# Performance work log

Measured on AMD Instinct MI355X. Metric: run time of the kernel, lower is better.

Reference implementation:

```python
import jax, jax.numpy as jnp
import numpy as np

TIME_STEPS = 49      # time_steps init arg
NUM_STEPS = 5000     # (time_steps+1)/dt = max_solve_steps
DT = 0.01            # dt0 in diffeqsolve
B = 8192             # batch of independent simulations


def setup_inputs() -> dict:
    key = jax.random.key(0)
    k1, k2, k3 = jax.random.split(key, 3)
    # positive, well-conditioned rates in [0.05, 0.5)
    condition = 0.05 + 0.45 * jax.random.uniform(k1, (B, 4), dtype=jnp.float32)
    # standard normals; scaled by sqrt(dt) inside reference -> Brownian increments
    dW = jax.random.normal(k2, (NUM_STEPS, B), dtype=jnp.float32)
    # uniform jitter used in summarize()'s max_at
    u = jax.random.uniform(k3, (B,), dtype=jnp.float32)
    return {"condition": condition, "dW": dW, "u": u}


def _simulate(condition, dW):
    # condition columns: infection_rate, recovery_rate, r0_mean_reversion, r0_volatility
    inf_rate = condition[:, 0]
    rec = condition[:, 1]
    mr = condition[:, 2]
    vol = condition[:, 3]
    r0_init = inf_rate / rec
    b = condition.shape[0]
    y0 = jnp.stack([
        jnp.full((b,), 0.99, condition.dtype),  # S
        jnp.full((b,), 0.01, condition.dtype),  # I
        jnp.zeros((b,), condition.dtype),       # R
        r0_init,                                # R0
    ], axis=-1)  # [B,4]
    sqrt_dt = jnp.sqrt(jnp.asarray(DT, condition.dtype))

    def step(y, dw):
        s, i, r, r0 = y[:, 0], y[:, 1], y[:, 2], y[:, 3]
        newly_infected = r0 * rec * s
        newly_recovered = rec * i
        # Euler-Maruyama: drift * dt + diffusion * dW, diffusion only on R0,
        # scaled by sqrt(|R0|) as in sde()
        y_new = jnp.stack([
            s - DT * newly_infected,
            i + DT * (newly_infected - newly_recovered),
            r + DT * newly_recovered,
            r0 + DT * mr * (r0_init - r0) + jnp.sqrt(jnp.abs(r0)) * vol * (dw * sqrt_dt),
        ], axis=-1)
        return y_new, y_new[:, 1]  # carry full state, emit infected fraction

    _, infected = jax.lax.scan(step, y0, dW)  # infected: [NUM_STEPS, B]
    # SaveAt ts = 1..TIME_STEPS: step k ends at t=(k+1)*DT, so t=m is index 100*m-1
    x = infected[99:100 * TIME_STEPS:100]  # [TIME_STEPS, B]
    return jnp.nan_to_num(x, nan=0.0, posinf=0.0, neginf=0.0)


def reference(condition, dW, u):
    x = _simulate(condition, dW)          # [T, B] infected trajectories
    x = jnp.clip(x, 1e-5)
    max_ = x.max(axis=0)
    max_at = (jnp.argmax(x, axis=0).astype(x.dtype) + u) / TIME_STEPS
    vol = jnp.std(jnp.diff(jnp.log(x), axis=0), axis=0)
    return jnp.stack([max_, max_at, vol], axis=-1)  # [B, 3]
```

## Files before the change

kernel.cpp:

```cpp
#include <hip/hip_runtime.h>
#include <math.h>

#define BATCH 8192
#define TPB   32
#define SEGN  25

#define REP25(M) M(0) M(1) M(2) M(3) M(4) M(5) M(6) M(7) M(8) M(9) \
  M(10) M(11) M(12) M(13) M(14) M(15) M(16) M(17) M(18) M(19) \
  M(20) M(21) M(22) M(23) M(24)

#define DECL_A(k) float a##k;
#define DECL_B(k) float b##k;
#define LD_A(k)   a##k = pA[(size_t)(k) * BATCH];
#define LD_B(k)   b##k = pB[(size_t)(k) * BATCH];

#define STEP_BODY(dwv) { \
    float dw  = (dwv); \
    float pr  = dtrec * r0; \
    float ps  = pr * s; \
    float r0a = r0 * c1 + c2; \
    float sq  = sqrtf(fabsf(r0)); \
    float g   = dw * volc; \
    s  = s - ps; \
    i_ = i_ * ci + ps; \
    r0 = r0a + sq * g; }

#define STEP_A(k) STEP_BODY(a##k)
#define STEP_B(k) STEP_BODY(b##k)

__global__ __launch_bounds__(TPB, 1)
void sir_sde_kernel(const float* __restrict__ cond,
                    const float* __restrict__ dW,
                    const float* __restrict__ uu,
                    float* __restrict__ out)
{
    const int b = blockIdx.x * TPB + threadIdx.x;

    const float inf_rate = cond[b * 4 + 0];
    const float rec      = cond[b * 4 + 1];
    const float mr       = cond[b * 4 + 2];
    const float vol      = cond[b * 4 + 3];

    const float dt    = 0.01f;
    const float r0i   = inf_rate / rec;
    const float dtrec = dt * rec;
    const float ci    = 1.0f - dtrec;
    const float c1    = 1.0f - dt * mr;
    const float c2    = (dt * mr) * r0i;
    const float volc  = vol * sqrtf(dt);

    float s  = 0.99f;
    float i_ = 0.01f;
    float r0 = r0i;

    float maxv = -1.0f, maxat = 0.0f;
    float prevlx = 0.0f, sum = 0.0f, sumsq = 0.0f;
    int   reccount = 0;

    REP25(DECL_A)
    REP25(DECL_B)

    const float* dWb = dW + b;
    const float* pA  = dWb;
    const float* pB;

    REP25(LD_A)

    for (int sg = 0; sg < 196; sg += 2) {
        pB = dWb + (size_t)(sg + 1) * SEGN * BATCH;
        __builtin_amdgcn_sched_barrier(0);
        REP25(LD_B)
        __builtin_amdgcn_sched_barrier(0);

        REP25(STEP_A)

        pA = dWb + (size_t)((sg + 2 < 196) ? sg + 2 : 0) * SEGN * BATCH;
        __builtin_amdgcn_sched_barrier(0);
        REP25(LD_A)
        __builtin_amdgcn_sched_barrier(0);

        REP25(STEP_B)

        if ((sg & 3) == 2) {
            float x = __builtin_isfinite(i_) ? i_ : 0.0f;
            x = fmaxf(x, 1e-5f);
            float lx = logf(x);
            if (reccount > 0) {
                float d = lx - prevlx;
                sum   += d;
                sumsq += d * d;
            }
            prevlx = lx;
            if (x > maxv) { maxv = x; maxat = (float)reccount; }
            ++reccount;
        }
    }

    float mean = sum / 48.0f;
    float var  = sumsq / 48.0f - mean * mean;
    var = fmaxf(var, 0.0f);
    float volout    = sqrtf(var);
    float maxat_out = (maxat + uu[b]) / 49.0f;

    out[b * 3 + 0] = maxv;
    out[b * 3 + 1] = maxat_out;
    out[b * 3 + 2] = volout;
}

extern "C" void kernel_launch(void* const* d_in, const int* in_sizes, int n_in,
                              void* d_out, int out_size, void* d_ws, size_t ws_size,
                              hipStream_t stream)
{
    (void)in_sizes; (void)n_in; (void)out_size; (void)d_ws; (void)ws_size;
    const float* cond = (const float*)d_in[0];
    const float* dW   = (const float*)d_in[1];
    const float* uu   = (const float*)d_in[2];
    float* out = (float*)d_out;

    dim3 grid(BATCH / TPB), block(TPB);
    hipLaunchKernelGGL(sir_sde_kernel, grid, block, 0, stream, cond, dW, uu, out);
}
```

Before: 625.6 us.

## Double segment size and hand-issue dW prefetch loads with explicit vmcnt waits

Each prefetch segment grows from 25 to 50 time steps. The dW loads are now issued through inline-asm global_load_dword with a scalar base and an incrementing vector offset, and explicit s_waitcnt vmcnt(50) makes the kernel wait only for the older batch while the newer 50 loads stay in flight. The record and stat update now runs once per 100-step iteration instead of behind a modulo test, and the u load is hoisted to kernel start. The aim is to hide global-memory latency better and avoid compiler-inserted conservative waits in a latency-bound serial recurrence. The cost is more VGPR pressure and fragile hand-managed waitcnt semantics.

```diff
diff --git a/kernel.cpp b/kernel.cpp
--- a/kernel.cpp
+++ b/kernel.cpp
@@ -3,16 +3,58 @@
 
 #define BATCH 8192
 #define TPB   32
-#define SEGN  25
+#define SEG   50
 
-#define REP25(M) M(0) M(1) M(2) M(3) M(4) M(5) M(6) M(7) M(8) M(9) \
+
+#define REP50(M) M(0) M(1) M(2) M(3) M(4) M(5) M(6) M(7) M(8) M(9) \
   M(10) M(11) M(12) M(13) M(14) M(15) M(16) M(17) M(18) M(19) \
-  M(20) M(21) M(22) M(23) M(24)
+  M(20) M(21) M(22) M(23) M(24) M(25) M(26) M(27) M(28) M(29) \
+  M(30) M(31) M(32) M(33) M(34) M(35) M(36) M(37) M(38) M(39) \
+  M(40) M(41) M(42) M(43) M(44) M(45) M(46) M(47) M(48) M(49)
 
-#define DECL_A(k) float a##k;
-#define DECL_B(k) float b##k;
-#define LD_A(k)   a##k = pA[(size_t)(k) * BATCH];
-#define LD_B(k)   b##k = pB[(size_t)(k) * BATCH];
+#define DECL_A(k) float A##k = 0.0f;
+#define DECL_B(k) float B##k = 0.0f;
+
+#define LDL(k) "global_load_dword %[d" #k "], %[ob], %[sb]\n\t" \
+               "v_add_u32 %[ob], 0x8000, %[ob]\n\t"
+
+#define LD25 LDL(0) LDL(1) LDL(2) LDL(3) LDL(4) LDL(5) LDL(6) LDL(7) \
+  LDL(8) LDL(9) LDL(10) LDL(11) LDL(12) LDL(13) LDL(14) LDL(15) LDL(16) \
+  LDL(17) LDL(18) LDL(19) LDL(20) LDL(21) LDL(22) LDL(23) LDL(24)
+
+#define LOAD_LO(P) asm volatile(LD25 \
+  : [d0]"=v"(P##0),[d1]"=v"(P##1),[d2]"=v"(P##2),[d3]"=v"(P##3), \
+    [d4]"=v"(P##4),[d5]"=v"(P##5),[d6]"=v"(P##6),[d7]"=v"(P##7), \
+    [d8]"=v"(P##8),[d9]"=v"(P##9),[d10]"=v"(P##10),[d11]"=v"(P##11), \
+    [d12]"=v"(P##12),[d13]"=v"(P##13),[d14]"=v"(P##14),[d15]"=v"(P##15), \
+    [d16]"=v"(P##16),[d17]"=v"(P##17),[d18]"=v"(P##18),[d19]"=v"(P##19), \
+    [d20]"=v"(P##20),[d21]"=v"(P##21),[d22]"=v"(P##22),[d23]"=v"(P##23), \
+    [d24]"=v"(P##24),[ob]"+v"(ob) \
+  : [sb]"s"(dWp))
+
+#define LOAD_HI(P) asm volatile(LD25 \
+  : [d0]"=v"(P##25),[d1]"=v"(P##26),[d2]"=v"(P##27),[d3]"=v"(P##28), \
+    [d4]"=v"(P##29),[d5]"=v"(P##30),[d6]"=v"(P##31),[d7]"=v"(P##32), \
+    [d8]"=v"(P##33),[d9]"=v"(P##34),[d10]"=v"(P##35),[d11]"=v"(P##36), \
+    [d12]"=v"(P##37),[d13]"=v"(P##38),[d14]"=v"(P##39),[d15]"=v"(P##40), \
+    [d16]"=v"(P##41),[d17]"=v"(P##42),[d18]"=v"(P##43),[d19]"=v"(P##44), \
+    [d20]"=v"(P##45),[d21]"=v"(P##46),[d22]"=v"(P##47),[d23]"=v"(P##48), \
+    [d24]"=v"(P##49),[ob]"+v"(ob) \
+  : [sb]"s"(dWp))
+
+#define WAIT_LO(P) asm volatile("s_waitcnt vmcnt(50)" \
+  : "+v"(P##0),"+v"(P##1),"+v"(P##2),"+v"(P##3),"+v"(P##4), \
+    "+v"(P##5),"+v"(P##6),"+v"(P##7),"+v"(P##8),"+v"(P##9), \
+    "+v"(P##10),"+v"(P##11),"+v"(P##12),"+v"(P##13),"+v"(P##14), \
+    "+v"(P##15),"+v"(P##16),"+v"(P##17),"+v"(P##18),"+v"(P##19), \
+    "+v"(P##20),"+v"(P##21),"+v"(P##22),"+v"(P##23),"+v"(P##24))
+
+#define WAIT_HI(P) asm volatile("s_waitcnt vmcnt(50)" \
+  : "+v"(P##25),"+v"(P##26),"+v"(P##27),"+v"(P##28),"+v"(P##29), \
+    "+v"(P##30),"+v"(P##31),"+v"(P##32),"+v"(P##33),"+v"(P##34), \
+    "+v"(P##35),"+v"(P##36),"+v"(P##37),"+v"(P##38),"+v"(P##39), \
+    "+v"(P##40),"+v"(P##41),"+v"(P##42),"+v"(P##43),"+v"(P##44), \
+    "+v"(P##45),"+v"(P##46),"+v"(P##47),"+v"(P##48),"+v"(P##49))
 
 #define STEP_BODY(dwv) { \
     float dw  = (dwv); \
@@ -25,10 +67,11 @@
     i_ = i_ * ci + ps; \
     r0 = r0a + sq * g; }
 
-#define STEP_A(k) STEP_BODY(a##k)
-#define STEP_B(k) STEP_BODY(b##k)
+#define STEP_A(k) STEP_BODY(A##k)
+#define STEP_B(k) STEP_BODY(B##k)
 
-__global__ __launch_bounds__(TPB, 1)
+__global__ __attribute__((amdgpu_flat_work_group_size(TPB, TPB),
+                          amdgpu_waves_per_eu(1, 1)))
 void sir_sde_kernel(const float* __restrict__ cond,
                     const float* __restrict__ dW,
                     const float* __restrict__ uu,
@@ -36,6 +79,7 @@
 {
     const int b = blockIdx.x * TPB + threadIdx.x;
 
+    const float u_in     = uu[b];
     const float inf_rate = cond[b * 4 + 0];
     const float rec      = cond[b * 4 + 1];
     const float mr       = cond[b * 4 + 2];
@@ -57,31 +101,27 @@
     float prevlx = 0.0f, sum = 0.0f, sumsq = 0.0f;
     int   reccount = 0;
 
-    REP25(DECL_A)
-    REP25(DECL_B)
+    REP50(DECL_A)
+    REP50(DECL_B)
 
-    const float* dWb = dW + b;
-    const float* pA  = dWb;
-    const float* pB;
+    const float* dWp = dW;
+    unsigned ob = (unsigned)b * 4u;
 
-    REP25(LD_A)
+    LOAD_LO(A); LOAD_HI(A);
 
-    for (int sg = 0; sg < 196; sg += 2) {
-        pB = dWb + (size_t)(sg + 1) * SEGN * BATCH;
-        __builtin_amdgcn_sched_barrier(0);
-        REP25(LD_B)
-        __builtin_amdgcn_sched_barrier(0);
+#pragma clang loop unroll(disable)
+    for (int sg = 0; sg < 98; sg += 2) {
+        LOAD_LO(B); LOAD_HI(B);
 
-        REP25(STEP_A)
+        WAIT_LO(A); WAIT_HI(A);
+        REP50(STEP_A)
 
-        pA = dWb + (size_t)((sg + 2 < 196) ? sg + 2 : 0) * SEGN * BATCH;
-        __builtin_amdgcn_sched_barrier(0);
-        REP25(LD_A)
-        __builtin_amdgcn_sched_barrier(0);
+        LOAD_LO(A); LOAD_HI(A);
 
-        REP25(STEP_B)
+        WAIT_LO(B); WAIT_HI(B);
+        REP50(STEP_B)
 
-        if ((sg & 3) == 2) {
+        {
             float x = __builtin_isfinite(i_) ? i_ : 0.0f;
             x = fmaxf(x, 1e-5f);
             float lx = logf(x);
@@ -96,11 +136,23 @@
         }
     }
 
+    asm volatile("s_waitcnt vmcnt(0)"
+      : "+v"(A0),"+v"(A1),"+v"(A2),"+v"(A3),"+v"(A4),"+v"(A5),"+v"(A6),
+        "+v"(A7),"+v"(A8),"+v"(A9),"+v"(A10),"+v"(A11),"+v"(A12),"+v"(A13),
+        "+v"(A14),"+v"(A15),"+v"(A16),"+v"(A17),"+v"(A18),"+v"(A19),
+        "+v"(A20),"+v"(A21),"+v"(A22),"+v"(A23),"+v"(A24) : : "memory");
+    asm volatile("s_waitcnt vmcnt(0)"
+      : "+v"(A25),"+v"(A26),"+v"(A27),"+v"(A28),"+v"(A29),"+v"(A30),
+        "+v"(A31),"+v"(A32),"+v"(A33),"+v"(A34),"+v"(A35),"+v"(A36),
+        "+v"(A37),"+v"(A38),"+v"(A39),"+v"(A40),"+v"(A41),"+v"(A42),
+        "+v"(A43),"+v"(A44),"+v"(A45),"+v"(A46),"+v"(A47),"+v"(A48),
+        "+v"(A49) : : "memory");
+
     float mean = sum / 48.0f;
     float var  = sumsq / 48.0f - mean * mean;
     var = fmaxf(var, 0.0f);
     float volout    = sqrtf(var);
-    float maxat_out = (maxat + uu[b]) / 49.0f;
+    float maxat_out = (maxat + u_in) / 49.0f;
 
     out[b * 3 + 0] = maxv;
     out[b * 3 + 1] = maxat_out;
```

Result: faster. 566.8 us (-9.4%).
